# Kernel tuning notes

Measured on AMD Instinct MI355X. Metric: run time of the kernel, lower is better.

## Reference

```python
import jax, jax.numpy as jnp
import numpy as np

N, E, D, B = 40000, 100000, 64, 256

def setup_inputs() -> dict:
    key = jax.random.key(0)
    ks = jax.random.split(key, 32)
    p = lambda k, shp: jax.random.normal(k, shp, dtype=jnp.float32) * 0.1
    inp = {
        'n_feat': jax.random.normal(ks[0], (N, 23), dtype=jnp.float32),
        'e_feat': jax.random.normal(ks[1], (E, 19), dtype=jnp.float32),
        'src': jax.random.randint(ks[2], (E,), 0, N, dtype=jnp.int32),
        'dst': jax.random.randint(ks[3], (E,), 0, N, dtype=jnp.int32),
        'node_graph': jnp.sort(jax.random.randint(ks[4], (N,), 0, B, dtype=jnp.int32)),
        'batch_size': B,
        'lin0_w': p(ks[5], (D, 23)), 'lin0_b': p(ks[6], (D,)),
        'en_w1': p(ks[7], (128, 19)), 'en_b1': p(ks[8], (128,)),
        'en_w2': p(ks[9], (D * D, 128)), 'en_b2': p(ks[10], (D * D,)),
        'conv_b': p(ks[11], (D,)),
        'gru_wih': p(ks[12], (3 * D, D)), 'gru_whh': p(ks[13], (3 * D, D)),
        'gru_bih': p(ks[14], (3 * D,)), 'gru_bhh': p(ks[15], (3 * D,)),
        'ls_wih0': p(ks[16], (4 * D, 2 * D)), 'ls_wih12': p(ks[17], (2, 4 * D, D)),
        'ls_whh': p(ks[18], (3, 4 * D, D)),
        'ls_bih': p(ks[19], (3, 4 * D)), 'ls_bhh': p(ks[20], (3, 4 * D)),
        'lin3_w': p(ks[21], (2 * D, 2 * D)), 'lin3_b': p(ks[22], (2 * D,)),
        'pred_w': p(ks[23], (1, 2 * D)), 'pred_b': p(ks[24], (1,)),
    }
    return inp


def _gru_step(x, h, wih, whh, bih, bhh):
    gi = x @ wih.T + bih   # (N, 3D)
    gh = h @ whh.T + bhh
    i_r, i_z, i_n = jnp.split(gi, 3, axis=-1)
    h_r, h_z, h_n = jnp.split(gh, 3, axis=-1)
    r = jax.nn.sigmoid(i_r + h_r)
    z = jax.nn.sigmoid(i_z + h_z)
    n = jnp.tanh(i_n + r * h_n)
    return (1.0 - z) * n + z * h


def _lstm_cell(x, h, c, wih, whh, bih, bhh):
    g = x @ wih.T + bih + h @ whh.T + bhh  # (B, 4D)
    i, f, gg, o = jnp.split(g, 4, axis=-1)
    c2 = jax.nn.sigmoid(f) * c + jax.nn.sigmoid(i) * jnp.tanh(gg)
    h2 = jax.nn.sigmoid(o) * jnp.tanh(c2)
    return h2, c2


def reference(n_feat, e_feat, src, dst, node_graph, batch_size,
              lin0_w, lin0_b, en_w1, en_b1, en_w2, en_b2, conv_b,
              gru_wih, gru_whh, gru_bih, gru_bhh,
              ls_wih0, ls_wih12, ls_whh, ls_bih, ls_bhh,
              lin3_w, lin3_b, pred_w, pred_b):
    d = lin0_b.shape[0]
    n_nodes = n_feat.shape[0]
    # input projection
    out = n_feat @ lin0_w.T + lin0_b                       # (N, D)
    h = out                                                # GRU hidden (1 layer)
    # edge network (same every step) -> per-edge weight matrices
    ew = jax.nn.relu(e_feat @ en_w1.T + en_b1) @ en_w2.T + en_b2
    ew = ew.reshape(-1, d, d)                              # (E, D, D)
    for _ in range(6):
        msg = jnp.einsum('ed,edf->ef', out[src], ew)       # gather + per-edge GEMM
        m = jax.ops.segment_sum(msg, dst, num_segments=n_nodes) + conv_b
        h = _gru_step(m, h, gru_wih, gru_whh, gru_bih, gru_bhh)
        out = h
    # Set2Set pooling
    hs = [jnp.zeros((batch_size, d), jnp.float32) for _ in range(3)]
    cs = [jnp.zeros((batch_size, d), jnp.float32) for _ in range(3)]
    q_star = jnp.zeros((batch_size, 2 * d), jnp.float32)
    for _ in range(6):
        x = q_star
        for l in range(3):
            wih = ls_wih0 if l == 0 else ls_wih12[l - 1]
            hs[l], cs[l] = _lstm_cell(x, hs[l], cs[l], wih, ls_whh[l], ls_bih[l], ls_bhh[l])
            x = hs[l]
        q = x                                              # (B, D)
        e = jnp.sum(out * q[node_graph], axis=-1)          # (N,)
        emax = jax.ops.segment_max(e, node_graph, num_segments=batch_size)
        ee = jnp.exp(e - emax[node_graph])
        esum = jax.ops.segment_sum(ee, node_graph, num_segments=batch_size)
        alpha = (ee / esum[node_graph])[:, None]
        readout = jax.ops.segment_sum(out * alpha, node_graph, num_segments=batch_size)
        q_star = jnp.concatenate([q, readout], axis=-1)
    y = jax.nn.relu(q_star @ lin3_w.T + lin3_b)
    predict = y @ pred_w.T + pred_b
    return h[None], predict
```

## Files before the change

kernel.cpp:

```cpp
#include <hip/hip_runtime.h>

typedef unsigned short u16;
typedef unsigned int u32;
typedef _Float16 f16;
typedef __attribute__((ext_vector_type(8))) _Float16 f16x8;
typedef __attribute__((ext_vector_type(4))) _Float16 f16x4;
typedef __attribute__((ext_vector_type(4))) float f32x4;

#define NN 40000
#define EE 100000
#define DD 64
#define BB 256
#define XTS 136
#define EPB 128

__device__ inline float sigmoidf_(float x){
    return 1.f / (1.f + __expf(-x));
}
__device__ inline float tanhf_(float x){
    x = fmaxf(fminf(x, 15.f), -15.f);
    float e = __expf(2.f * x);
    return (e - 1.f) / (e + 1.f);
}

typedef __attribute__((address_space(3))) unsigned int lds_u32;
typedef __attribute__((address_space(1))) const unsigned int g_u32;
__device__ inline void gload_lds16(const void* g, void* l){
    __builtin_amdgcn_global_load_lds((g_u32*)g, (lds_u32*)l, 16, 0, 0);
}

__global__ __launch_bounds__(256) void prep_kernel(
    const float* __restrict__ en_w2, f16* __restrict__ w2h,
    const float* __restrict__ gru_wih, const float* __restrict__ gru_whh,
    f16* __restrict__ wf16h, f16* __restrict__ wf16l,
    const float* __restrict__ ls_wih0, const float* __restrict__ ls_wih12,
    const float* __restrict__ ls_whh, float* __restrict__ lsT,
    const float* __restrict__ lin3_w, float* __restrict__ lin3T,
    const float* __restrict__ gru_bih, const float* __restrict__ conv_b,
    float* __restrict__ effb,
    const int* __restrict__ node_graph, int* __restrict__ offs)
{
    int i = blockIdx.x * 256 + threadIdx.x;
    if (i < 524288){
        w2h[i] = (f16)en_w2[i];
        return;
    }
    i -= 524288;
    if (i < 49152){
        int sel = i / 12288;
        int r = i % 12288;
        int gg = sel >> 1, islo = sel & 1;
        float v = (gg ? gru_whh : gru_wih)[r];
        f16 hi = (f16)v;
        if (islo) wf16l[gg * 12288 + r] = (f16)(v - (float)hi);
        else      wf16h[gg * 12288 + r] = hi;
        return;
    }
    i -= 49152;
    if (i < 114688){
        float v;
        if (i < 32768){
            int d = i >> 8, g = i & 255;
            v = ls_wih0[g * 128 + d];
        } else if (i < 65536){
            int j = i - 32768;
            int l = j >> 14, r = j & 16383;
            int d = r >> 8, g = r & 255;
            v = ls_wih12[l * 16384 + g * 64 + d];
        } else {
            int j = i - 65536;
            int l = j >> 14, r = j & 16383;
            int d = r >> 8, g = r & 255;
            v = ls_whh[l * 16384 + g * 64 + d];
        }
        lsT[i] = v;
        return;
    }
    i -= 114688;
    if (i < 16384){
        int ii = i >> 7, jj = i & 127;
        lin3T[i] = lin3_w[jj * 128 + ii];
        return;
    }
    i -= 16384;
    if (i < 192){
        float b = gru_bih[i];
        #pragma unroll
        for (int d = 0; d < 64; d++) b += gru_wih[i * 64 + d] * conv_b[d];
        effb[i] = b;
        return;
    }
    i -= 192;
    if (i <= 256){
        int lo = 0, hi = NN;
        while (lo < hi){
            int mid = (lo + hi) >> 1;
            if (node_graph[mid] < i) lo = mid + 1; else hi = mid;
        }
        offs[i] = lo;
        return;
    }
}

__global__ __launch_bounds__(256) void lin0_kernel(
    const float* __restrict__ nf, const float* __restrict__ w,
    const float* __restrict__ b, float* __restrict__ out)
{
    int tid = blockIdx.x * 256 + threadIdx.x;
    int n = tid >> 6, d = tid & 63;
    if (n >= NN) return;
    float acc = b[d];
    const float* nr = nf + (size_t)n * 23;
    const float* wr = w + d * 23;
    #pragma unroll
    for (int j = 0; j < 23; j++) acc = fmaf(nr[j], wr[j], acc);
    out[(size_t)n * 64 + d] = acc;
}

__global__ __launch_bounds__(256) void edge_hidden_kernel(
    const float* __restrict__ ef, const float* __restrict__ w1,
    const float* __restrict__ b1, f16* __restrict__ hidh)
{
    int tid = blockIdx.x * 256 + threadIdx.x;
    int e = tid >> 7, k = tid & 127;
    if (e >= EE) return;
    float acc = b1[k];
    const float* er = ef + (size_t)e * 19;
    const float* wr = w1 + k * 19;
    #pragma unroll
    for (int j = 0; j < 19; j++) acc = fmaf(er[j], wr[j], acc);
    acc = fmaxf(acc, 0.f);
    hidh[(size_t)e * 128 + k] = (f16)acc;
}

__global__ __launch_bounds__(512) void msg_fused_kernel(
    const float* __restrict__ h, const f16* __restrict__ hidh,
    const f16* __restrict__ w2h, const float* __restrict__ b2,
    const int* __restrict__ src, const int* __restrict__ dst,
    float* __restrict__ m)
{
    __shared__ f16 s_xT[64 * XTS];
    __shared__ int s_dst[EPB];
    __shared__ f16x8 s_bb[2][1024];

    const int t = threadIdx.x;
    const int base = blockIdx.x * EPB;
    const int lane = t & 63;
    const int wid = t >> 6;

    int goff[2], lbase[2];
    #pragma unroll
    for (int cc = 0; cc < 2; cc++){
        int s = cc * 512 + wid * 64 + lane;
        int kh = s >> 9;
        int c2 = s & 511;
        int col = c2 >> 3;
        int jj = (c2 & 7) ^ (col & 7);
        goff[cc] = col * 128 + kh * 64 + jj * 8;
        lbase[cc] = cc * 512 + wid * 64;
    }

#define STG_ISSUE(DN, BUF)                                                   \
    {                                                                        \
        const f16* gsrc = w2h + (size_t)(DN) * 8192;                         \
        gload_lds16(gsrc + goff[0], &s_bb[BUF][lbase[0]]);                   \
        gload_lds16(gsrc + goff[1], &s_bb[BUF][lbase[1]]);                   \
    }

    STG_ISSUE(0, 0);

    for (int i = t; i < EPB * 64; i += 512){
        int el = i >> 6, f = i & 63;
        int e = base + el;
        float v = 0.f;
        if (e < EE) v = h[(size_t)src[e] * 64 + f];
        s_xT[f * XTS + el] = (f16)v;
    }
    if (t < EPB){
        int e = base + t;
        s_dst[t] = (e < EE) ? dst[e] : -1;
    }

    const int eg = wid >> 1;
    const int fp = wid & 1;
    const int r16 = lane & 15;
    const int kg = lane >> 4;
    const int we = eg * 32;
    const int sw = r16 & 7;

    f16x8 ah[2][4];
    #pragma unroll
    for (int mt = 0; mt < 2; mt++){
        int e = base + we + mt * 16 + r16;
        #pragma unroll
        for (int ks = 0; ks < 4; ks++){
            if (e < EE){
                ah[mt][ks] = *(const f16x8*)(hidh + (size_t)e * 128 + ks * 32 + kg * 8);
            } else {
                f16x8 z = {0,0,0,0,0,0,0,0};
                ah[mt][ks] = z;
            }
        }
    }

    f32x4 msg[2][2];
    #pragma unroll
    for (int a = 0; a < 2; a++)
        #pragma unroll
        for (int b = 0; b < 2; b++){
            f32x4 z = {0.f, 0.f, 0.f, 0.f};
            msg[a][b] = z;
        }

    int rslot[2][4];
    #pragma unroll
    for (int ftl = 0; ftl < 2; ftl++){
        int col = fp * 32 + ftl * 16 + r16;
        #pragma unroll
        for (int ks = 0; ks < 4; ks++){
            int j2 = (ks & 1) * 4 + kg;
            rslot[ftl][ks] = (ks >> 1) * 512 + col * 8 + (j2 ^ sw);
        }
    }

    __syncthreads();

    for (int d = 0; d < 64; d++){
        int cur = d & 1;
        if (d < 63) STG_ISSUE(d + 1, cur ^ 1);
        f32x4 xv[2];
        #pragma unroll
        for (int mt = 0; mt < 2; mt++){
            f16x4 xh = *(const f16x4*)&s_xT[d * XTS + we + mt * 16 + kg * 4];
            #pragma unroll
            for (int r = 0; r < 4; r++) xv[mt][r] = (float)xh[r];
        }
        __builtin_amdgcn_s_setprio(1);
        #pragma unroll
        for (int ftl = 0; ftl < 2; ftl++){
            f16x8 bf0 = s_bb[cur][rslot[ftl][0]];
            f16x8 bf1 = s_bb[cur][rslot[ftl][1]];
            f16x8 bf2 = s_bb[cur][rslot[ftl][2]];
            f16x8 bf3 = s_bb[cur][rslot[ftl][3]];
            float b2v = b2[d * 64 + fp * 32 + ftl * 16 + r16];
            #pragma unroll
            for (int mt = 0; mt < 2; mt++){
                f32x4 acc = {b2v, b2v, b2v, b2v};
                acc = __builtin_amdgcn_mfma_f32_16x16x32_f16(ah[mt][0], bf0, acc, 0, 0, 0);
                acc = __builtin_amdgcn_mfma_f32_16x16x32_f16(ah[mt][1], bf1, acc, 0, 0, 0);
                acc = __builtin_amdgcn_mfma_f32_16x16x32_f16(ah[mt][2], bf2, acc, 0, 0, 0);
                acc = __builtin_amdgcn_mfma_f32_16x16x32_f16(ah[mt][3], bf3, acc, 0, 0, 0);
                msg[mt][ftl] = xv[mt] * acc + msg[mt][ftl];
            }
        }
        __builtin_amdgcn_s_setprio(0);
        __syncthreads();
    }
#undef STG_ISSUE

    #pragma unroll
    for (int mt = 0; mt < 2; mt++){
        #pragma unroll
        for (int r = 0; r < 4; r++){
            int el = we + mt * 16 + kg * 4 + r;
            int dt = s_dst[el];
            if (dt >= 0){
                #pragma unroll
                for (int ftl = 0; ftl < 2; ftl++)
                    atomicAdd(&m[(size_t)dt * 64 + fp * 32 + ftl * 16 + r16],
                              msg[mt][ftl][r]);
            }
        }
    }
}

__global__ __launch_bounds__(256) void gru_mfma_kernel(
    float* __restrict__ m, float* __restrict__ h,
    const f16* __restrict__ wf16h, const f16* __restrict__ wf16l,
    const float* __restrict__ effb, const float* __restrict__ bhh)
{
    __shared__ float s_g[2][32][194];
    const int t = threadIdx.x;
    const int base = blockIdx.x * 32;
    const int lane = t & 63;
    const int wid = t >> 6;
    const int rt = wid & 1;
    const int gg = wid >> 1;
    const int r16 = lane & 15;
    const int kg = lane >> 4;

    const float* __restrict__ X = gg ? h : m;
    int n = base + rt * 16 + r16;

    f16x8 ah[2], al[2];
    #pragma unroll
    for (int ks = 0; ks < 2; ks++){
        const float* xp = X + (size_t)n * 64 + ks * 32 + kg * 8;
        f32x4 v0 = *(const f32x4*)(xp);
        f32x4 v1 = *(const f32x4*)(xp + 4);
        #pragma unroll
        for (int j = 0; j < 4; j++){
            f16 hi0 = (f16)v0[j], hi1 = (f16)v1[j];
            ah[ks][j] = hi0;     ah[ks][4 + j] = hi1;
            al[ks][j] = (f16)(v0[j] - (float)hi0);
            al[ks][4 + j] = (f16)(v1[j] - (float)hi1);
        }
    }

    const f16* __restrict__ wh = wf16h + gg * 12288;
    const f16* __restrict__ wl = wf16l + gg * 12288;
    #pragma unroll
    for (int ct = 0; ct < 12; ct++){
        int g = ct * 16 + r16;
        f16x8 bh0 = *(const f16x8*)(wh + g * 64 + kg * 8);
        f16x8 bh1 = *(const f16x8*)(wh + g * 64 + 32 + kg * 8);
        f16x8 bl0 = *(const f16x8*)(wl + g * 64 + kg * 8);
        f16x8 bl1 = *(const f16x8*)(wl + g * 64 + 32 + kg * 8);
        f32x4 acc = {0.f, 0.f, 0.f, 0.f};
        acc = __builtin_amdgcn_mfma_f32_16x16x32_f16(ah[0], bh0, acc, 0, 0, 0);
        acc = __builtin_amdgcn_mfma_f32_16x16x32_f16(ah[1], bh1, acc, 0, 0, 0);
        acc = __builtin_amdgcn_mfma_f32_16x16x32_f16(ah[0], bl0, acc, 0, 0, 0);
        acc = __builtin_amdgcn_mfma_f32_16x16x32_f16(ah[1], bl1, acc, 0, 0, 0);
        acc = __builtin_amdgcn_mfma_f32_16x16x32_f16(al[0], bh0, acc, 0, 0, 0);
        acc = __builtin_amdgcn_mfma_f32_16x16x32_f16(al[1], bh1, acc, 0, 0, 0);
        #pragma unroll
        for (int r = 0; r < 4; r++)
            s_g[gg][rt * 16 + kg * 4 + r][ct * 16 + r16] = acc[r];
    }
    __syncthreads();

    int node = t >> 3;
    int f0 = (t & 7) * 8;
    int n2 = base + node;
    #pragma unroll
    for (int j = 0; j < 8; j++){
        int f = f0 + j;
        float gir = s_g[0][node][f]       + effb[f];
        float giz = s_g[0][node][64 + f]  + effb[64 + f];
        float gin = s_g[0][node][128 + f] + effb[128 + f];
        float ghr = s_g[1][node][f]       + bhh[f];
        float ghz = s_g[1][node][64 + f]  + bhh[64 + f];
        float ghn = s_g[1][node][128 + f] + bhh[128 + f];
        float r = sigmoidf_(gir + ghr);
        float z = sigmoidf_(giz + ghz);
        float nv = tanhf_(gin + r * ghn);
        size_t hb = (size_t)n2 * 64 + f;
        float hv = h[hb];
        h[hb] = (1.f - z) * nv + z * hv;
        m[hb] = 0.f;
    }
}

__global__ __launch_bounds__(256) void set2set_kernel(
    const float* __restrict__ out, const int* __restrict__ offs,
    const float* __restrict__ lsT, const float* __restrict__ ls_bih,
    const float* __restrict__ ls_bhh, const float* __restrict__ lin3T,
    const float* __restrict__ lin3_b, const float* __restrict__ pred_w,
    const float* __restrict__ pred_b, float* __restrict__ e_ws,
    float* __restrict__ pred_out)
{
    int g = blockIdx.x;
    int t = threadIdx.x;
    int ln = t >> 6, d = t & 63;
    __shared__ float s_qstar[128], s_h[3][64], s_c[3][64], s_g[256];
    __shared__ float s_r[4][64], s_red[4], s_wsum[4], s_y[128];
    if (t < 128) s_qstar[t] = 0.f;
    if (t < 192){ s_h[t / 64][t % 64] = 0.f; s_c[t / 64][t % 64] = 0.f; }
    int ns = offs[g], ne = offs[g + 1];
    __syncthreads();

#define LSTM_GATE(L)                                                         \
    __syncthreads();                                                         \
    s_g[t] = acc;                                                            \
    __syncthreads();                                                         \
    if (t < 64){                                                             \
        float iv = s_g[t], fv = s_g[64 + t], gv = s_g[128 + t], ov = s_g[192 + t]; \
        float c2 = sigmoidf_(fv) * s_c[L][t] + sigmoidf_(iv) * tanhf_(gv);   \
        float h2 = sigmoidf_(ov) * tanhf_(c2);                               \
        s_c[L][t] = c2; s_h[L][t] = h2;                                      \
    }                                                                        \
    __syncthreads();

    for (int it = 0; it < 6; it++){
        {
            float acc = ls_bih[t] + ls_bhh[t];
            const float* wx = lsT;
            #pragma unroll 32
            for (int j = 0; j < 128; j++) acc = fmaf(s_qstar[j], wx[j * 256 + t], acc);
            const float* wh = lsT + 65536;
            #pragma unroll 32
            for (int j = 0; j < 64; j++) acc = fmaf(s_h[0][j], wh[j * 256 + t], acc);
            LSTM_GATE(0)
        }
        {
            float acc = ls_bih[256 + t] + ls_bhh[256 + t];
            const float* wx = lsT + 32768;
            #pragma unroll 32
            for (int j = 0; j < 64; j++) acc = fmaf(s_h[0][j], wx[j * 256 + t], acc);
            const float* wh = lsT + 65536 + 16384;
            #pragma unroll 32
            for (int j = 0; j < 64; j++) acc = fmaf(s_h[1][j], wh[j * 256 + t], acc);
            LSTM_GATE(1)
        }
        {
            float acc = ls_bih[512 + t] + ls_bhh[512 + t];
            const float* wx = lsT + 32768 + 16384;
            #pragma unroll 32
            for (int j = 0; j < 64; j++) acc = fmaf(s_h[1][j], wx[j * 256 + t], acc);
            const float* wh = lsT + 65536 + 2 * 16384;
            #pragma unroll 32
            for (int j = 0; j < 64; j++) acc = fmaf(s_h[2][j], wh[j * 256 + t], acc);
            LSTM_GATE(2)
        }
        float wmax = -3.4e38f;
        #pragma unroll 2
        for (int n = ns + ln; n < ne; n += 4){
            float p = out[(size_t)n * 64 + d] * s_h[2][d];
            #pragma unroll
            for (int o = 1; o < 64; o <<= 1) p += __shfl_xor(p, o);
            if (d == 0) e_ws[n] = p;
            wmax = fmaxf(wmax, p);
        }
        if (d == 0) s_red[ln] = wmax;
        __syncthreads();
        float gmax = fmaxf(fmaxf(s_red[0], s_red[1]), fmaxf(s_red[2], s_red[3]));
        float wsum = 0.f, racc = 0.f;
        #pragma unroll 2
        for (int n = ns + ln; n < ne; n += 4){
            float w = __expf(e_ws[n] - gmax);
            wsum += w;
            racc = fmaf(w, out[(size_t)n * 64 + d], racc);
        }
        s_r[ln][d] = racc;
        if (d == 0) s_wsum[ln] = wsum;
        __syncthreads();
        if (t < 64){
            float gsum = s_wsum[0] + s_wsum[1] + s_wsum[2] + s_wsum[3];
            float ro = s_r[0][t] + s_r[1][t] + s_r[2][t] + s_r[3][t];
            ro = (gsum > 0.f) ? ro / gsum : 0.f;
            s_qstar[t] = s_h[2][t];
            s_qstar[64 + t] = ro;
        }
        __syncthreads();
    }
#undef LSTM_GATE
    if (t < 128){
        float acc = lin3_b[t];
        #pragma unroll 32
        for (int i = 0; i < 128; i++) acc = fmaf(s_qstar[i], lin3T[i * 128 + t], acc);
        s_y[t] = fmaxf(acc, 0.f);
    }
    __syncthreads();
    if (t < 64){
        float p = s_y[t] * pred_w[t] + s_y[64 + t] * pred_w[64 + t];
        #pragma unroll
        for (int o = 1; o < 64; o <<= 1) p += __shfl_xor(p, o);
        if (t == 0) pred_out[g] = p + pred_b[0];
    }
}

extern "C" void kernel_launch(void* const* d_in, const int* in_sizes, int n_in,
                              void* d_out, int out_size, void* d_ws, size_t ws_size,
                              hipStream_t stream)
{
    (void)in_sizes; (void)n_in; (void)out_size; (void)ws_size;
    const float* n_feat  = (const float*)d_in[0];
    const float* e_feat  = (const float*)d_in[1];
    const int*   src     = (const int*)d_in[2];
    const int*   dst     = (const int*)d_in[3];
    const int*   node_graph = (const int*)d_in[4];
    const float* lin0_w  = (const float*)d_in[6];
    const float* lin0_b  = (const float*)d_in[7];
    const float* en_w1   = (const float*)d_in[8];
    const float* en_b1   = (const float*)d_in[9];
    const float* en_w2   = (const float*)d_in[10];
    const float* en_b2   = (const float*)d_in[11];
    const float* conv_b  = (const float*)d_in[12];
    const float* gru_wih = (const float*)d_in[13];
    const float* gru_whh = (const float*)d_in[14];
    const float* gru_bih = (const float*)d_in[15];
    const float* gru_bhh = (const float*)d_in[16];
    const float* ls_wih0 = (const float*)d_in[17];
    const float* ls_wih12= (const float*)d_in[18];
    const float* ls_whh  = (const float*)d_in[19];
    const float* ls_bih  = (const float*)d_in[20];
    const float* ls_bhh  = (const float*)d_in[21];
    const float* lin3_w  = (const float*)d_in[22];
    const float* lin3_b  = (const float*)d_in[23];
    const float* pred_w  = (const float*)d_in[24];
    const float* pred_b  = (const float*)d_in[25];

    float* h = (float*)d_out;
    float* pred_out = (float*)d_out + (size_t)NN * 64;

    char* ws = (char*)d_ws;
    f16*   hidh  = (f16*)(ws + 0);
    float* m     = (float*)(ws + 25600000);
    f16*   w2h   = (f16*)(ws + 35840000);
    f16*   wf16h = (f16*)(ws + 36888576);
    f16*   wf16l = (f16*)(ws + 36937728);
    float* lsT   = (float*)(ws + 36986880);
    float* lin3T = (float*)(ws + 37445632);
    float* effb  = (float*)(ws + 37511168);
    float* e_ws  = (float*)(ws + 37511936);
    int*   offs  = (int*)(ws + 37671936);

    prep_kernel<<<2754, 256, 0, stream>>>(en_w2, w2h, gru_wih, gru_whh,
                                          wf16h, wf16l,
                                          ls_wih0, ls_wih12, ls_whh, lsT,
                                          lin3_w, lin3T, gru_bih, conv_b, effb,
                                          node_graph, offs);
    lin0_kernel<<<(NN * 64) / 256, 256, 0, stream>>>(n_feat, lin0_w, lin0_b, h);
    edge_hidden_kernel<<<(EE * 128) / 256, 256, 0, stream>>>(e_feat, en_w1, en_b1, hidh);
    hipMemsetAsync(m, 0, (size_t)NN * 64 * sizeof(float), stream);

    for (int step = 0; step < 6; step++){
        msg_fused_kernel<<<(EE + EPB - 1) / EPB, 512, 0, stream>>>(h, hidh, w2h,
                                                                   en_b2, src, dst, m);
        gru_mfma_kernel<<<NN / 32, 256, 0, stream>>>(m, h, wf16h, wf16l, effb, gru_bhh);
    }

    set2set_kernel<<<BB, 256, 0, stream>>>(h, offs, lsT, ls_bih, ls_bhh,
                                           lin3T, lin3_b, pred_w, pred_b,
                                           e_ws, pred_out);
}
```

Measured before the change: 1.373 ms.

## Triple-buffer w2 tile staging with partial vmcnt waits and stage bias in LDS

Replaces the double-buffered async global-to-LDS staging of the edge-network weight slices in the message kernel with a three-deep ring. The ring prefetches two slices ahead and waits with explicit vmcnt counts and a raw barrier instead of a full __syncthreads. The b2 bias is preloaded into LDS as fp16 rather than read from global memory each iteration. The aim is to hide global load latency behind MFMA work. In exchange it uses more LDS, which may lower occupancy, and rounds the bias to fp16.

```diff
diff --git a/kernel.cpp b/kernel.cpp
--- a/kernel.cpp
+++ b/kernel.cpp
@@ -140,8 +140,9 @@
     float* __restrict__ m)
 {
     __shared__ f16 s_xT[64 * XTS];
+    __shared__ f16 s_b2f[4096];
     __shared__ int s_dst[EPB];
-    __shared__ f16x8 s_bb[2][1024];
+    __shared__ f16x8 s_t0[1024], s_t1[1024], s_t2[1024];
 
     const int t = threadIdx.x;
     const int base = blockIdx.x * EPB;
@@ -163,11 +164,15 @@
 #define STG_ISSUE(DN, BUF)                                                   \
     {                                                                        \
         const f16* gsrc = w2h + (size_t)(DN) * 8192;                         \
-        gload_lds16(gsrc + goff[0], &s_bb[BUF][lbase[0]]);                   \
-        gload_lds16(gsrc + goff[1], &s_bb[BUF][lbase[1]]);                   \
-    }
-
-    STG_ISSUE(0, 0);
+        gload_lds16(gsrc + goff[0], (BUF) + lbase[0]);                       \
+        gload_lds16(gsrc + goff[1], (BUF) + lbase[1]);                       \
+    }
+
+    f16x8* pb0 = s_t0;
+    f16x8* pb1 = s_t1;
+    f16x8* pb2 = s_t2;
+    STG_ISSUE(0, pb0);
+    STG_ISSUE(1, pb1);
 
     for (int i = t; i < EPB * 64; i += 512){
         int el = i >> 6, f = i & 63;
@@ -176,6 +181,7 @@
         if (e < EE) v = h[(size_t)src[e] * 64 + f];
         s_xT[f * XTS + el] = (f16)v;
     }
+    for (int i = t; i < 4096; i += 512) s_b2f[i] = (f16)b2[i];
     if (t < EPB){
         int e = base + t;
         s_dst[t] = (e < EE) ? dst[e] : -1;
@@ -226,8 +232,7 @@
     __syncthreads();
 
     for (int d = 0; d < 64; d++){
-        int cur = d & 1;
-        if (d < 63) STG_ISSUE(d + 1, cur ^ 1);
+        if (d + 2 < 64) STG_ISSUE(d + 2, pb2);
         f32x4 xv[2];
         #pragma unroll
         for (int mt = 0; mt < 2; mt++){
@@ -238,11 +243,11 @@
         __builtin_amdgcn_s_setprio(1);
         #pragma unroll
         for (int ftl = 0; ftl < 2; ftl++){
-            f16x8 bf0 = s_bb[cur][rslot[ftl][0]];
-            f16x8 bf1 = s_bb[cur][rslot[ftl][1]];
-            f16x8 bf2 = s_bb[cur][rslot[ftl][2]];
-            f16x8 bf3 = s_bb[cur][rslot[ftl][3]];
-            float b2v = b2[d * 64 + fp * 32 + ftl * 16 + r16];
+            f16x8 bf0 = pb0[rslot[ftl][0]];
+            f16x8 bf1 = pb0[rslot[ftl][1]];
+            f16x8 bf2 = pb0[rslot[ftl][2]];
+            f16x8 bf3 = pb0[rslot[ftl][3]];
+            float b2v = (float)s_b2f[d * 64 + fp * 32 + ftl * 16 + r16];
             #pragma unroll
             for (int mt = 0; mt < 2; mt++){
                 f32x4 acc = {b2v, b2v, b2v, b2v};
@@ -254,7 +259,12 @@
             }
         }
         __builtin_amdgcn_s_setprio(0);
-        __syncthreads();
+        if (d < 63){
+            if (d <= 61) asm volatile("s_waitcnt vmcnt(2)" ::: "memory");
+            else         asm volatile("s_waitcnt vmcnt(0)" ::: "memory");
+            __builtin_amdgcn_s_barrier();
+        }
+        f16x8* tmp = pb0; pb0 = pb1; pb1 = pb2; pb2 = tmp;
     }
 #undef STG_ISSUE
 
```

New measurement: 1.269 ms. 1.08x faster.
